# Kernel optimization log

Hardware: AMD Instinct MI355X
Metric: run time of the kernel (lower is better)

Reference implementation:

```python
import jax, jax.numpy as jnp
import numpy as np
import math

B, N, D, H = 2, 64, 256, 8
DK = D // H


def setup_inputs() -> dict:
    key = jax.random.key(0)
    ks = jax.random.split(key, 12)
    s = 1.0 / math.sqrt(D)
    inp = {
        "state": jax.random.normal(ks[0], (B, N, N, D), dtype=jnp.float32),
        "mask": jnp.zeros((B, N, N, N), dtype=bool),
        "W_lk": jax.random.normal(ks[1], (D, D), dtype=jnp.float32) * s,
        "b_lk": jnp.zeros((D,), dtype=jnp.float32),
        "W_rk": jax.random.normal(ks[2], (D, D), dtype=jnp.float32) * s,
        "b_rk": jnp.zeros((D,), dtype=jnp.float32),
        "W_lv": jax.random.normal(ks[3], (D, D), dtype=jnp.float32) * s,
        "b_lv": jnp.zeros((D,), dtype=jnp.float32),
        "W_rv": jax.random.normal(ks[4], (D, D), dtype=jnp.float32) * s,
        "b_rv": jnp.zeros((D,), dtype=jnp.float32),
        "W_o": jax.random.normal(ks[5], (D, D), dtype=jnp.float32) * s,
        "b_o": jnp.zeros((D,), dtype=jnp.float32),
    }
    return inp


def _proj(x, W, b):
    # torch nn.Linear: x @ W.T + b, then view to heads
    y = jnp.einsum('bxyd,ed->bxye', x, W) + b
    return y.reshape(B, N, N, H, DK)


def reference(state, mask, W_lk, b_lk, W_rk, b_rk, W_lv, b_lv, W_rv, b_rv, W_o, b_o):
    left_k = _proj(state, W_lk, b_lk)   # [B,N,N,H,DK]
    right_k = _proj(state, W_rk, b_rk)
    left_v = _proj(state, W_lv, b_lv)
    right_v = _proj(state, W_rv, b_rv)

    # triangle-style scores over node triples (x, a, y): [B,N,N,N,H]
    scores = jnp.einsum('bxahd,bayhd->bxayh', left_k, right_k) / math.sqrt(DK)
    scores = jnp.where(mask[..., None], jnp.float32(-1000.0), scores)
    att = jax.nn.softmax(scores, axis=2)  # softmax over intermediate node a

    # val[b,x,a,y,h,d] = left_v[b,x,a,h,d] * right_v[b,a,y,h,d] (materialized as in torch)
    val = jnp.einsum('bxahd,bayhd->bxayhd', left_v, right_v)
    x = jnp.einsum('bxayh,bxayhd->bxyhd', att, val)  # sum over a
    x = x.reshape(B, N, N, D)
    return jnp.einsum('bxyd,ed->bxye', x, W_o) + b_o
```

## Files before the change

### kernel.cpp

```cpp
#include <hip/hip_runtime.h>

#define B 2
#define N 64
#define D 256
#define H 8
#define DK 32
#define M (B * N * N)

typedef __attribute__((ext_vector_type(8))) short bf16x8;
typedef __attribute__((ext_vector_type(4))) float f32x4;

#define OFF_LK 0
#define OFF_RK 256
#define OFF_LV 512
#define OFF_RV 768

__device__ __forceinline__ ushort f2b(float f) {
    union { float f; unsigned u; } v; v.f = f;
    unsigned r = v.u + 0x7fffu + ((v.u >> 16) & 1u);
    return (ushort)(r >> 16);
}
__device__ __forceinline__ float b2f(ushort u) {
    union { unsigned u; float f; } v; v.u = ((unsigned)u) << 16; return v.f;
}
__device__ __forceinline__ void cvt8(float4 raw, float* f) {
    const ushort* s = (const ushort*)&raw;
#pragma unroll
    for (int j = 0; j < 8; ++j) f[j] = b2f(s[j]);
}

__device__ __forceinline__ void glds16(const ushort* g, ushort* l) {
    __builtin_amdgcn_global_load_lds(
        (const __attribute__((address_space(1))) unsigned int*)g,
        (__attribute__((address_space(3))) unsigned int*)l, 16, 0, 0);
}

__global__ __launch_bounds__(256) void cast_all(const float* __restrict__ state,
                                                const float* __restrict__ W_lk, const float* __restrict__ W_rk,
                                                const float* __restrict__ W_lv, const float* __restrict__ W_rv,
                                                const float* __restrict__ W_o,
                                                const float* __restrict__ b_lk, const float* __restrict__ b_rk,
                                                const float* __restrict__ b_lv, const float* __restrict__ b_rv,
                                                const float* __restrict__ b_o,
                                                ushort* __restrict__ state_bf,
                                                ushort* __restrict__ Wcat,
                                                float* __restrict__ bias_cat) {
    const int gid = blockIdx.x * 256 + threadIdx.x;
    const float* Ws[5] = {W_lk, W_rk, W_lv, W_rv, W_o};
    const float* bs[5] = {b_lk, b_rk, b_lv, b_rv, b_o};

    if (gid < 1280) bias_cat[gid] = bs[gid >> 8][gid & 255];

    if (gid < 524288) {
        float4 v = *(const float4*)&state[(size_t)gid * 4];
        ushort4 o = {f2b(v.x), f2b(v.y), f2b(v.z), f2b(v.w)};
        *(ushort4*)&state_bf[(size_t)gid * 4] = o;
    } else {
        int u = gid - 524288;
        int row = u >> 6;
        int k4 = (u & 63) * 4;
        const float* W = Ws[row >> 8];
        float4 v = *(const float4*)&W[(size_t)(row & 255) * 256 + k4];
        ushort4 o = {f2b(v.x), f2b(v.y), f2b(v.z), f2b(v.w)};
        *(ushort4*)&Wcat[(size_t)row * 256 + k4] = o;
    }
}

template <int BF16OUT>
__global__ __launch_bounds__(256) void gemm_mfma(const ushort* __restrict__ A,
                                                 const ushort* __restrict__ Bw,
                                                 const float* __restrict__ bias,
                                                 void* __restrict__ Cv, int ldc) {
    __shared__ __align__(16) ushort As[128 * 32];
    __shared__ __align__(16) ushort Bs[128 * 32];
    const int tid = threadIdx.x;
    const int lane = tid & 63;
    const int wave = tid >> 6;
    const int wm = (wave & 1) * 64;
    const int wn = (wave >> 1) * 64;
    const int row0 = blockIdx.x * 128;
    const int col0 = blockIdx.y * 128;

    const int lr = lane >> 2;
    const int lkq = (lane & 3) * 8;

    const ushort* gA0 = A + (size_t)(row0 + wave * 32 + lr) * 256 + lkq;
    const ushort* gA1 = gA0 + 16 * 256;
    const ushort* gB0 = Bw + (size_t)(col0 + wave * 32 + lr) * 256 + lkq;
    const ushort* gB1 = gB0 + 16 * 256;
    ushort* lA0 = &As[(wave * 32) * 32];
    ushort* lA1 = &As[(wave * 32 + 16) * 32];
    ushort* lB0 = &Bs[(wave * 32) * 32];
    ushort* lB1 = &Bs[(wave * 32 + 16) * 32];

    const int fr = lane & 15;
    const int fk = (lane >> 4) * 8;

    f32x4 acc[4][4] = {};

    for (int k0 = 0; k0 < 256; k0 += 32) {
        __syncthreads();
        glds16(gA0 + k0, lA0);
        glds16(gA1 + k0, lA1);
        glds16(gB0 + k0, lB0);
        glds16(gB1 + k0, lB1);
        __syncthreads();

        bf16x8 af[4], bf[4];
#pragma unroll
        for (int i = 0; i < 4; ++i)
            af[i] = *(const bf16x8*)&As[(wm + i * 16 + fr) * 32 + fk];
#pragma unroll
        for (int j = 0; j < 4; ++j)
            bf[j] = *(const bf16x8*)&Bs[(wn + j * 16 + fr) * 32 + fk];
#pragma unroll
        for (int i = 0; i < 4; ++i)
#pragma unroll
            for (int j = 0; j < 4; ++j)
                acc[i][j] = __builtin_amdgcn_mfma_f32_16x16x32_bf16(af[i], bf[j], acc[i][j], 0, 0, 0);
    }

#pragma unroll
    for (int j = 0; j < 4; ++j) {
        const int col = col0 + wn + j * 16 + (lane & 15);
        const float bv = bias[col];
#pragma unroll
        for (int i = 0; i < 4; ++i) {
            const int rbase = row0 + wm + i * 16 + (lane >> 4) * 4;
#pragma unroll
            for (int r = 0; r < 4; ++r) {
                float o = acc[i][j][r] + bv;
                if (BF16OUT) ((ushort*)Cv)[(size_t)(rbase + r) * ldc + col] = f2b(o);
                else ((float*)Cv)[(size_t)(rbase + r) * ldc + col] = o;
            }
        }
    }
}

__global__ __launch_bounds__(256) void scores_kernel(const ushort* __restrict__ P,
                                                     const unsigned char* __restrict__ mask,
                                                     ushort* __restrict__ att) {
    const int a = blockIdx.x, h = blockIdx.y, b = blockIdx.z;
    __shared__ __align__(16) float LKs[DK][68];
    __shared__ __align__(16) float RKs[DK][68];
    const int tid = threadIdx.x;

    {
        const int x = tid >> 2;
        const int d0 = (tid & 3) * 8;
        float f[8];
        float4 v = *(const float4*)&P[(((size_t)b * N + x) * N + a) * 1024 + OFF_LK + h * DK + d0];
        cvt8(v, f);
#pragma unroll
        for (int j = 0; j < 8; ++j) LKs[d0 + j][x] = f[j];
        float4 w = *(const float4*)&P[(((size_t)b * N + a) * N + x) * 1024 + OFF_RK + h * DK + d0];
        cvt8(w, f);
#pragma unroll
        for (int j = 0; j < 8; ++j) RKs[d0 + j][x] = f[j];
    }
    __syncthreads();

    const int tx = tid & 15, ty = tid >> 4;
    float acc[4][4] = {};
#pragma unroll
    for (int d = 0; d < DK; ++d) {
        float4 xa = *(const float4*)&LKs[d][ty * 4];
        float4 yb = *(const float4*)&RKs[d][tx * 4];
        acc[0][0] += xa.x * yb.x; acc[0][1] += xa.x * yb.y; acc[0][2] += xa.x * yb.z; acc[0][3] += xa.x * yb.w;
        acc[1][0] += xa.y * yb.x; acc[1][1] += xa.y * yb.y; acc[1][2] += xa.y * yb.z; acc[1][3] += xa.y * yb.w;
        acc[2][0] += xa.z * yb.x; acc[2][1] += xa.z * yb.y; acc[2][2] += xa.z * yb.z; acc[2][3] += xa.z * yb.w;
        acc[3][0] += xa.w * yb.x; acc[3][1] += xa.w * yb.y; acc[3][2] += xa.w * yb.z; acc[3][3] += xa.w * yb.w;
    }

    const float scale = 0.17677669529663687f;
    ushort* tile = &att[(((size_t)(b * H + h) * N + a) * N) * N];
#pragma unroll
    for (int i = 0; i < 4; ++i) {
        const int x = ty * 4 + i;
        uchar4 mk = *(const uchar4*)&mask[(((size_t)b * N + x) * N + a) * N + tx * 4];
        ushort4 o;
        o.x = f2b(mk.x ? -1000.0f : acc[i][0] * scale);
        o.y = f2b(mk.y ? -1000.0f : acc[i][1] * scale);
        o.z = f2b(mk.z ? -1000.0f : acc[i][2] * scale);
        o.w = f2b(mk.w ? -1000.0f : acc[i][3] * scale);
        *(ushort4*)&tile[x * 64 + tx * 4] = o;
    }
}

__global__ __launch_bounds__(256) void combine_kernel(const ushort* __restrict__ P,
                                                      const ushort* __restrict__ att,
                                                      ushort* __restrict__ xbuf) {
    __shared__ __align__(16) float2 LVs2[8 * 16 * 16];
    __shared__ __align__(16) float2 RVs2[8 * 16 * 18];
    __shared__ __align__(16) float atts[16 * 164];
    __shared__ float mstate[16][17];
    __shared__ float lstate[16][17];
    __shared__ float alphas[16][17];

    const int bh = blockIdx.z;
    const int b = bh >> 3, h = bh & 7;
    const int x0 = blockIdx.x * 16, y0 = blockIdx.y * 16;
    const int tid = threadIdx.x;
    const int x_l = tid >> 4, dp = tid & 15;

    mstate[x_l][dp] = -3.0e38f;
    lstate[x_l][dp] = 0.0f;

    float2 acc[16] = {};

    for (int ac = 0; ac < N; ac += 8) {
        __syncthreads();
        {
            const int r = tid >> 1, q = tid & 1;
            float f[16];
            {
                int x = r >> 3, a = r & 7;
                const ushort* src = &P[(((size_t)b * N + x0 + x) * N + ac + a) * 1024 + OFF_LV + h * DK + q * 16];
                cvt8(*(const float4*)&src[0], f);
                cvt8(*(const float4*)&src[8], f + 8);
                float2* dst = &LVs2[(a * 16 + x) * 16 + q * 8];
#pragma unroll
                for (int j = 0; j < 4; ++j)
                    *(float4*)&dst[2 * j] = make_float4(f[4 * j], f[4 * j + 1], f[4 * j + 2], f[4 * j + 3]);
            }
            {
                int a = r >> 4, y = r & 15;
                const ushort* src = &P[(((size_t)b * N + ac + a) * N + y0 + y) * 1024 + OFF_RV + h * DK + q * 16];
                cvt8(*(const float4*)&src[0], f);
                cvt8(*(const float4*)&src[8], f + 8);
#pragma unroll
                for (int m2 = 0; m2 < 8; ++m2)
                    RVs2[(a * 16 + q * 8 + m2) * 18 + y] = make_float2(f[2 * m2], f[2 * m2 + 1]);
            }
            {
                int x = r >> 3, a = r & 7;
                const ushort* src = &att[(((size_t)bh * N + ac + a) * N + x0 + x) * N + y0 + q * 8];
                cvt8(*(const float4*)&src[0], f);
                float* dst = &atts[x * 164 + a * 20 + q * 8];
                *(float4*)&dst[0] = make_float4(f[0], f[1], f[2], f[3]);
                *(float4*)&dst[4] = make_float4(f[4], f[5], f[6], f[7]);
            }
        }
        __syncthreads();

        {
            const int sx = x_l, sy = dp;
            float s8[8];
#pragma unroll
            for (int a = 0; a < 8; ++a) s8[a] = atts[sx * 164 + a * 20 + sy];
            float mc = s8[0];
#pragma unroll
            for (int a = 1; a < 8; ++a) mc = fmaxf(mc, s8[a]);
            const float mold = mstate[sx][sy];
            const float mnew = fmaxf(mold, mc);
            const float alpha = __expf(mold - mnew);
            float ps = 0.0f;
#pragma unroll
            for (int a = 0; a < 8; ++a) {
                float p = __expf(s8[a] - mnew);
                atts[sx * 164 + a * 20 + sy] = p;
                ps += p;
            }
            lstate[sx][sy] = lstate[sx][sy] * alpha + ps;
            mstate[sx][sy] = mnew;
            alphas[sx][sy] = alpha;
        }
        __syncthreads();

#pragma unroll
        for (int y = 0; y < 16; ++y) {
            float al = alphas[x_l][y];
            acc[y].x *= al; acc[y].y *= al;
        }

#pragma unroll
        for (int a = 0; a < 8; ++a) {
            float2 lv = LVs2[(a * 16 + x_l) * 16 + dp];
            const float* wrow = &atts[x_l * 164 + a * 20];
            const float2* rvrow = &RVs2[(a * 16 + dp) * 18];
            float4 wq[4];
#pragma unroll
            for (int j = 0; j < 4; ++j) wq[j] = *(const float4*)&wrow[j * 4];
            const float* wv = (const float*)wq;
#pragma unroll
            for (int yq = 0; yq < 8; ++yq) {
                float4 rv4 = *(const float4*)&rvrow[yq * 2];
                float w0 = wv[yq * 2], w1 = wv[yq * 2 + 1];
                acc[yq * 2].x += (w0 * lv.x) * rv4.x;
                acc[yq * 2].y += (w0 * lv.y) * rv4.y;
                acc[yq * 2 + 1].x += (w1 * lv.x) * rv4.z;
                acc[yq * 2 + 1].y += (w1 * lv.y) * rv4.w;
            }
        }
    }

#pragma unroll
    for (int y = 0; y < 16; ++y) {
        const float invl = 1.0f / lstate[x_l][y];
        ushort2 o = {f2b(acc[y].x * invl), f2b(acc[y].y * invl)};
        *(ushort2*)&xbuf[(((size_t)b * N + x0 + x_l) * N + y0 + y) * D + h * DK + 2 * dp] = o;
    }
}

extern "C" void kernel_launch(void* const* d_in, const int* in_sizes, int n_in,
                              void* d_out, int out_size, void* d_ws, size_t ws_size,
                              hipStream_t stream) {
    const float* state = (const float*)d_in[0];
    const unsigned char* mask = (const unsigned char*)d_in[1];
    const float* W_lk = (const float*)d_in[2];
    const float* b_lk = (const float*)d_in[3];
    const float* W_rk = (const float*)d_in[4];
    const float* b_rk = (const float*)d_in[5];
    const float* W_lv = (const float*)d_in[6];
    const float* b_lv = (const float*)d_in[7];
    const float* W_rv = (const float*)d_in[8];
    const float* b_rv = (const float*)d_in[9];
    const float* W_o = (const float*)d_in[10];
    const float* b_o = (const float*)d_in[11];
    float* out = (float*)d_out;

    char* ws = (char*)d_ws;
    ushort* P_bf = (ushort*)ws;
    ws += (size_t)M * 1024 * 2;
    ushort* att_bf = (ushort*)ws;
    ws += (size_t)B * H * N * N * N * 2;
    float* bias_cat = (float*)ws;
    ws += 1280 * 4;
    ushort* state_bf = (ushort*)ws;
    ws += (size_t)M * D * 2;
    ushort* Wcat = (ushort*)ws;
    ws += (size_t)1280 * 256 * 2;
    ushort* xbuf_bf = (ushort*)ws;

    cast_all<<<2368, 256, 0, stream>>>(state, W_lk, W_rk, W_lv, W_rv, W_o,
                                       b_lk, b_rk, b_lv, b_rv, b_o,
                                       state_bf, Wcat, bias_cat);
    gemm_mfma<1><<<dim3(M / 128, 8), 256, 0, stream>>>(state_bf, Wcat, bias_cat, P_bf, 1024);
    scores_kernel<<<dim3(N, H, B), 256, 0, stream>>>(P_bf, mask, att_bf);
    combine_kernel<<<dim3(4, 4, B * H), 256, 0, stream>>>(P_bf, att_bf, xbuf_bf);
    gemm_mfma<0><<<dim3(M / 128, 2), 256, 0, stream>>>(xbuf_bf, Wcat + 1024 * 256, bias_cat + 1024, out, 256);
}
```

Before: 140.0 us.

## Fuse score computation into combine kernel with MFMA scores and 4x4 register tiling

Merges the separate scores kernel into the online-softmax combine kernel, so each block computes its 16x16 score tiles per 8-wide chunk of the intermediate node with bf16 MFMA instructions. This removes the global round-trip of the B*H*N^3 bf16 attention tensor and one kernel launch. The combine inner loop is also re-tiled so each thread holds a 4x4 (x,y) block of accumulators, which raises register reuse of the LV/RV values loaded from shared memory. In exchange, each block adds an extra barrier and MFMA phase per chunk, and the grid stays at only 256 blocks.

```diff
diff --git a/kernel.cpp b/kernel.cpp
--- a/kernel.cpp
+++ b/kernel.cpp
@@ -137,168 +137,165 @@
     }
 }
 
-__global__ __launch_bounds__(256) void scores_kernel(const ushort* __restrict__ P,
-                                                     const unsigned char* __restrict__ mask,
-                                                     ushort* __restrict__ att) {
-    const int a = blockIdx.x, h = blockIdx.y, b = blockIdx.z;
-    __shared__ __align__(16) float LKs[DK][68];
-    __shared__ __align__(16) float RKs[DK][68];
-    const int tid = threadIdx.x;
-
-    {
-        const int x = tid >> 2;
-        const int d0 = (tid & 3) * 8;
-        float f[8];
-        float4 v = *(const float4*)&P[(((size_t)b * N + x) * N + a) * 1024 + OFF_LK + h * DK + d0];
-        cvt8(v, f);
-#pragma unroll
-        for (int j = 0; j < 8; ++j) LKs[d0 + j][x] = f[j];
-        float4 w = *(const float4*)&P[(((size_t)b * N + a) * N + x) * 1024 + OFF_RK + h * DK + d0];
-        cvt8(w, f);
-#pragma unroll
-        for (int j = 0; j < 8; ++j) RKs[d0 + j][x] = f[j];
-    }
-    __syncthreads();
-
-    const int tx = tid & 15, ty = tid >> 4;
-    float acc[4][4] = {};
-#pragma unroll
-    for (int d = 0; d < DK; ++d) {
-        float4 xa = *(const float4*)&LKs[d][ty * 4];
-        float4 yb = *(const float4*)&RKs[d][tx * 4];
-        acc[0][0] += xa.x * yb.x; acc[0][1] += xa.x * yb.y; acc[0][2] += xa.x * yb.z; acc[0][3] += xa.x * yb.w;
-        acc[1][0] += xa.y * yb.x; acc[1][1] += xa.y * yb.y; acc[1][2] += xa.y * yb.z; acc[1][3] += xa.y * yb.w;
-        acc[2][0] += xa.z * yb.x; acc[2][1] += xa.z * yb.y; acc[2][2] += xa.z * yb.z; acc[2][3] += xa.z * yb.w;
-        acc[3][0] += xa.w * yb.x; acc[3][1] += xa.w * yb.y; acc[3][2] += xa.w * yb.z; acc[3][3] += xa.w * yb.w;
-    }
-
-    const float scale = 0.17677669529663687f;
-    ushort* tile = &att[(((size_t)(b * H + h) * N + a) * N) * N];
-#pragma unroll
-    for (int i = 0; i < 4; ++i) {
-        const int x = ty * 4 + i;
-        uchar4 mk = *(const uchar4*)&mask[(((size_t)b * N + x) * N + a) * N + tx * 4];
-        ushort4 o;
-        o.x = f2b(mk.x ? -1000.0f : acc[i][0] * scale);
-        o.y = f2b(mk.y ? -1000.0f : acc[i][1] * scale);
-        o.z = f2b(mk.z ? -1000.0f : acc[i][2] * scale);
-        o.w = f2b(mk.w ? -1000.0f : acc[i][3] * scale);
-        *(ushort4*)&tile[x * 64 + tx * 4] = o;
-    }
-}
-
-__global__ __launch_bounds__(256) void combine_kernel(const ushort* __restrict__ P,
-                                                      const ushort* __restrict__ att,
-                                                      ushort* __restrict__ xbuf) {
-    __shared__ __align__(16) float2 LVs2[8 * 16 * 16];
-    __shared__ __align__(16) float2 RVs2[8 * 16 * 18];
-    __shared__ __align__(16) float atts[16 * 164];
-    __shared__ float mstate[16][17];
-    __shared__ float lstate[16][17];
-    __shared__ float alphas[16][17];
+__global__ __launch_bounds__(256) void fused_attn(const ushort* __restrict__ P,
+                                                  const unsigned char* __restrict__ mask,
+                                                  ushort* __restrict__ xbuf) {
+    __shared__ __align__(16) ushort LKs[8 * 16 * 40];
+    __shared__ __align__(16) ushort RKs[8 * 16 * 40];
+    __shared__ __align__(16) float2 LVs[8 * 16 * 18];
+    __shared__ __align__(16) float2 RVs[8 * 16 * 18];
+    __shared__ __align__(16) float atts[8 * 16 * 20];
+    __shared__ __align__(16) unsigned char masks[16 * 8 * 16];
+    __shared__ float mstate[16 * 20];
+    __shared__ float lstate[16 * 20];
+    __shared__ float alphas[16 * 20];
 
     const int bh = blockIdx.z;
     const int b = bh >> 3, h = bh & 7;
     const int x0 = blockIdx.x * 16, y0 = blockIdx.y * 16;
     const int tid = threadIdx.x;
-    const int x_l = tid >> 4, dp = tid & 15;
-
-    mstate[x_l][dp] = -3.0e38f;
-    lstate[x_l][dp] = 0.0f;
-
-    float2 acc[16] = {};
+    const int lane = tid & 63, wave = tid >> 6;
+
+    const int xg = tid >> 6, yg = (tid >> 4) & 3, dp = tid & 15;
+    const int sx = tid >> 4, sy = tid & 15;
+
+    mstate[sx * 20 + sy] = -3.0e38f;
+    lstate[sx * 20 + sy] = 0.0f;
+
+    float2 acc[4][4] = {};
+    const float scale = 0.17677669529663687f;
 
     for (int ac = 0; ac < N; ac += 8) {
         __syncthreads();
         {
             const int r = tid >> 1, q = tid & 1;
+            const int xs = r >> 3, as = r & 7;
+            const int ar = r >> 4, yr = r & 15;
+            {
+                const ushort* s = &P[(((size_t)b * N + x0 + xs) * N + ac + as) * 1024 + OFF_LK + h * DK + q * 16];
+                *(float4*)&LKs[(as * 16 + xs) * 40 + q * 16]     = *(const float4*)&s[0];
+                *(float4*)&LKs[(as * 16 + xs) * 40 + q * 16 + 8] = *(const float4*)&s[8];
+            }
+            {
+                const ushort* s = &P[(((size_t)b * N + ac + ar) * N + y0 + yr) * 1024 + OFF_RK + h * DK + q * 16];
+                *(float4*)&RKs[(ar * 16 + yr) * 40 + q * 16]     = *(const float4*)&s[0];
+                *(float4*)&RKs[(ar * 16 + yr) * 40 + q * 16 + 8] = *(const float4*)&s[8];
+            }
             float f[16];
             {
-                int x = r >> 3, a = r & 7;
-                const ushort* src = &P[(((size_t)b * N + x0 + x) * N + ac + a) * 1024 + OFF_LV + h * DK + q * 16];
-                cvt8(*(const float4*)&src[0], f);
-                cvt8(*(const float4*)&src[8], f + 8);
-                float2* dst = &LVs2[(a * 16 + x) * 16 + q * 8];
-#pragma unroll
-                for (int j = 0; j < 4; ++j)
-                    *(float4*)&dst[2 * j] = make_float4(f[4 * j], f[4 * j + 1], f[4 * j + 2], f[4 * j + 3]);
+                const ushort* s = &P[(((size_t)b * N + x0 + xs) * N + ac + as) * 1024 + OFF_LV + h * DK + q * 16];
+                cvt8(*(const float4*)&s[0], f);
+                cvt8(*(const float4*)&s[8], f + 8);
+#pragma unroll
+                for (int m2 = 0; m2 < 8; ++m2)
+                    LVs[(as * 16 + q * 8 + m2) * 18 + xs] = make_float2(f[2 * m2], f[2 * m2 + 1]);
             }
             {
-                int a = r >> 4, y = r & 15;
-                const ushort* src = &P[(((size_t)b * N + ac + a) * N + y0 + y) * 1024 + OFF_RV + h * DK + q * 16];
-                cvt8(*(const float4*)&src[0], f);
-                cvt8(*(const float4*)&src[8], f + 8);
+                const ushort* s = &P[(((size_t)b * N + ac + ar) * N + y0 + yr) * 1024 + OFF_RV + h * DK + q * 16];
+                cvt8(*(const float4*)&s[0], f);
+                cvt8(*(const float4*)&s[8], f + 8);
 #pragma unroll
                 for (int m2 = 0; m2 < 8; ++m2)
-                    RVs2[(a * 16 + q * 8 + m2) * 18 + y] = make_float2(f[2 * m2], f[2 * m2 + 1]);
-            }
-            {
-                int x = r >> 3, a = r & 7;
-                const ushort* src = &att[(((size_t)bh * N + ac + a) * N + x0 + x) * N + y0 + q * 8];
-                cvt8(*(const float4*)&src[0], f);
-                float* dst = &atts[x * 164 + a * 20 + q * 8];
-                *(float4*)&dst[0] = make_float4(f[0], f[1], f[2], f[3]);
-                *(float4*)&dst[4] = make_float4(f[4], f[5], f[6], f[7]);
+                    RVs[(ar * 16 + q * 8 + m2) * 18 + yr] = make_float2(f[2 * m2], f[2 * m2 + 1]);
+            }
+            if (tid < 128) {
+                const int xm = tid >> 3, am = tid & 7;
+                const unsigned char* s = &mask[(((size_t)b * N + x0 + xm) * N + ac + am) * N + y0];
+                *(int4*)&masks[(xm * 8 + am) * 16] = *(const int4*)s;
             }
         }
         __syncthreads();
 
         {
-            const int sx = x_l, sy = dp;
+            const int fr = lane & 15;
+            const int fkq = (lane >> 4) * 8;
+            const int yq = lane & 15, xq = (lane >> 4) * 4;
+#pragma unroll
+            for (int aw = 0; aw < 2; ++aw) {
+                const int a = wave * 2 + aw;
+                bf16x8 af = *(const bf16x8*)&LKs[(a * 16 + fr) * 40 + fkq];
+                bf16x8 bfv = *(const bf16x8*)&RKs[(a * 16 + fr) * 40 + fkq];
+                f32x4 s = {};
+                s = __builtin_amdgcn_mfma_f32_16x16x32_bf16(af, bfv, s, 0, 0, 0);
+#pragma unroll
+                for (int rr = 0; rr < 4; ++rr) {
+                    const int x = xq + rr;
+                    float sv = s[rr] * scale;
+                    if (masks[(x * 8 + a) * 16 + yq]) sv = -1000.0f;
+                    atts[(a * 16 + x) * 20 + yq] = sv;
+                }
+            }
+        }
+        __syncthreads();
+
+        {
             float s8[8];
 #pragma unroll
-            for (int a = 0; a < 8; ++a) s8[a] = atts[sx * 164 + a * 20 + sy];
+            for (int a = 0; a < 8; ++a) s8[a] = atts[(a * 16 + sx) * 20 + sy];
             float mc = s8[0];
 #pragma unroll
             for (int a = 1; a < 8; ++a) mc = fmaxf(mc, s8[a]);
-            const float mold = mstate[sx][sy];
+            const float mold = mstate[sx * 20 + sy];
             const float mnew = fmaxf(mold, mc);
             const float alpha = __expf(mold - mnew);
             float ps = 0.0f;
 #pragma unroll
             for (int a = 0; a < 8; ++a) {
                 float p = __expf(s8[a] - mnew);
-                atts[sx * 164 + a * 20 + sy] = p;
+                atts[(a * 16 + sx) * 20 + sy] = p;
                 ps += p;
             }
-            lstate[sx][sy] = lstate[sx][sy] * alpha + ps;
-            mstate[sx][sy] = mnew;
-            alphas[sx][sy] = alpha;
-        }
-        __syncthreads();
-
-#pragma unroll
-        for (int y = 0; y < 16; ++y) {
-            float al = alphas[x_l][y];
-            acc[y].x *= al; acc[y].y *= al;
-        }
-
-#pragma unroll
-        for (int a = 0; a < 8; ++a) {
-            float2 lv = LVs2[(a * 16 + x_l) * 16 + dp];
-            const float* wrow = &atts[x_l * 164 + a * 20];
-            const float2* rvrow = &RVs2[(a * 16 + dp) * 18];
-            float4 wq[4];
-#pragma unroll
-            for (int j = 0; j < 4; ++j) wq[j] = *(const float4*)&wrow[j * 4];
-            const float* wv = (const float*)wq;
-#pragma unroll
-            for (int yq = 0; yq < 8; ++yq) {
-                float4 rv4 = *(const float4*)&rvrow[yq * 2];
-                float w0 = wv[yq * 2], w1 = wv[yq * 2 + 1];
-                acc[yq * 2].x += (w0 * lv.x) * rv4.x;
-                acc[yq * 2].y += (w0 * lv.y) * rv4.y;
-                acc[yq * 2 + 1].x += (w1 * lv.x) * rv4.z;
-                acc[yq * 2 + 1].y += (w1 * lv.y) * rv4.w;
-            }
-        }
-    }
-
-#pragma unroll
-    for (int y = 0; y < 16; ++y) {
-        const float invl = 1.0f / lstate[x_l][y];
-        ushort2 o = {f2b(acc[y].x * invl), f2b(acc[y].y * invl)};
-        *(ushort2*)&xbuf[(((size_t)b * N + x0 + x_l) * N + y0 + y) * D + h * DK + 2 * dp] = o;
+            lstate[sx * 20 + sy] = lstate[sx * 20 + sy] * alpha + ps;
+            mstate[sx * 20 + sy] = mnew;
+            alphas[sx * 20 + sy] = alpha;
+        }
+        __syncthreads();
+
+        {
+#pragma unroll
+            for (int i = 0; i < 4; ++i) {
+                float4 av = *(const float4*)&alphas[(xg * 4 + i) * 20 + yg * 4];
+                const float* ap = (const float*)&av;
+#pragma unroll
+                for (int j = 0; j < 4; ++j) {
+                    acc[i][j].x *= ap[j];
+                    acc[i][j].y *= ap[j];
+                }
+            }
+#pragma unroll
+            for (int a = 0; a < 8; ++a) {
+                float4 lq0 = *(const float4*)&LVs[(a * 16 + dp) * 18 + xg * 4];
+                float4 lq1 = *(const float4*)&LVs[(a * 16 + dp) * 18 + xg * 4 + 2];
+                float4 rq0 = *(const float4*)&RVs[(a * 16 + dp) * 18 + yg * 4];
+                float4 rq1 = *(const float4*)&RVs[(a * 16 + dp) * 18 + yg * 4 + 2];
+                float2 lv[4] = {make_float2(lq0.x, lq0.y), make_float2(lq0.z, lq0.w),
+                                make_float2(lq1.x, lq1.y), make_float2(lq1.z, lq1.w)};
+                float2 rv[4] = {make_float2(rq0.x, rq0.y), make_float2(rq0.z, rq0.w),
+                                make_float2(rq1.x, rq1.y), make_float2(rq1.z, rq1.w)};
+#pragma unroll
+                for (int i = 0; i < 4; ++i) {
+                    float4 at = *(const float4*)&atts[(a * 16 + xg * 4 + i) * 20 + yg * 4];
+                    const float* wp = (const float*)&at;
+#pragma unroll
+                    for (int j = 0; j < 4; ++j) {
+                        acc[i][j].x += (wp[j] * lv[i].x) * rv[j].x;
+                        acc[i][j].y += (wp[j] * lv[i].y) * rv[j].y;
+                    }
+                }
+            }
+        }
+    }
+
+#pragma unroll
+    for (int i = 0; i < 4; ++i) {
+        float4 lq = *(const float4*)&lstate[(xg * 4 + i) * 20 + yg * 4];
+        const float* lp = (const float*)&lq;
+#pragma unroll
+        for (int j = 0; j < 4; ++j) {
+            const float invl = 1.0f / lp[j];
+            ushort2 o = {f2b(acc[i][j].x * invl), f2b(acc[i][j].y * invl)};
+            *(ushort2*)&xbuf[(((size_t)b * N + x0 + xg * 4 + i) * N + y0 + yg * 4 + j) * D + h * DK + 2 * dp] = o;
+        }
     }
 }
 
@@ -322,8 +319,6 @@
     char* ws = (char*)d_ws;
     ushort* P_bf = (ushort*)ws;
     ws += (size_t)M * 1024 * 2;
-    ushort* att_bf = (ushort*)ws;
-    ws += (size_t)B * H * N * N * N * 2;
     float* bias_cat = (float*)ws;
     ws += 1280 * 4;
     ushort* state_bf = (ushort*)ws;
@@ -336,7 +331,6 @@
                                        b_lk, b_rk, b_lv, b_rv, b_o,
                                        state_bf, Wcat, bias_cat);
     gemm_mfma<1><<<dim3(M / 128, 8), 256, 0, stream>>>(state_bf, Wcat, bias_cat, P_bf, 1024);
-    scores_kernel<<<dim3(N, H, B), 256, 0, stream>>>(P_bf, mask, att_bf);
-    combine_kernel<<<dim3(4, 4, B * H), 256, 0, stream>>>(P_bf, att_bf, xbuf_bf);
+    fused_attn<<<dim3(4, 4, B * H), 256, 0, stream>>>(P_bf, mask, xbuf_bf);
     gemm_mfma<0><<<dim3(M / 128, 2), 256, 0, stream>>>(xbuf_bf, Wcat + 1024 * 256, bias_cat + 1024, out, 256);
 }
```

New measurement: 133.7 us. 1.05x faster.
